# Optimization experiments

Measured on AMD Instinct MI355X. Metric: run time of the kernel, lower is better.

## Reference

```python
import jax, jax.numpy as jnp
import numpy as np

N = 50000
E = 800000
EPS = 1e-12


def sage_conv(x, src, dst, W_l, b_l, W_r):
    # PyG SAGEConv (mean aggr): out = lin_l(mean_{j in N(i)} x_j) + lin_r(x_i)
    msg = x[src]                                             # [E, d] gather
    agg = jax.ops.segment_sum(msg, dst, num_segments=N)      # [N, d]
    cnt = jax.ops.segment_sum(jnp.ones((E,), x.dtype), dst, num_segments=N)
    mean = agg / jnp.maximum(cnt, 1.0)[:, None]              # isolated nodes -> 0
    return mean @ W_l + b_l + x @ W_r


def setup_inputs() -> dict:
    key = jax.random.key(0)
    ks = jax.random.split(key, 12)
    s = 0.05
    return {
        "x": jax.random.normal(ks[0], (N, 128), dtype=jnp.float32),
        "edge_index": jax.random.randint(ks[1], (2, E), 0, N, dtype=jnp.int64),
        # pre: Linear(128 -> 128)
        "pre_W": jax.random.normal(ks[2], (128, 128), dtype=jnp.float32) * s,
        "pre_b": jnp.zeros((128,), dtype=jnp.float32),
        # conv_first: SAGEConv(128 -> 256)
        "W1_l": jax.random.normal(ks[3], (128, 256), dtype=jnp.float32) * s,
        "b1": jnp.zeros((256,), dtype=jnp.float32),
        "W1_r": jax.random.normal(ks[4], (128, 256), dtype=jnp.float32) * s,
        # conv_hidden[0]: SAGEConv(256 -> 256)
        "W2_l": jax.random.normal(ks[5], (256, 256), dtype=jnp.float32) * s,
        "b2": jnp.zeros((256,), dtype=jnp.float32),
        "W2_r": jax.random.normal(ks[6], (256, 256), dtype=jnp.float32) * s,
        # conv_out: SAGEConv(256 -> 256)
        "W3_l": jax.random.normal(ks[7], (256, 256), dtype=jnp.float32) * s,
        "b3": jnp.zeros((256,), dtype=jnp.float32),
        "W3_r": jax.random.normal(ks[8], (256, 256), dtype=jnp.float32) * s,
    }


def reference(x, edge_index, pre_W, pre_b, W1_l, b1, W1_r, W2_l, b2, W2_r, W3_l, b3, W3_r):
    src, dst = edge_index[0], edge_index[1]
    h = x @ pre_W + pre_b                                   # feature_pre Linear
    h = jax.nn.relu(sage_conv(h, src, dst, W1_l, b1, W1_r))  # dropout = identity (eval)
    h = jax.nn.relu(sage_conv(h, src, dst, W2_l, b2, W2_r))
    h = sage_conv(h, src, dst, W3_l, b3, W3_r)
    norm = jnp.sqrt(jnp.sum(h * h, axis=-1, keepdims=True))
    return h / jnp.maximum(norm, EPS)                       # F.normalize(p=2, dim=-1)
```

## Files before the change

### kernel.cpp

```cpp
#include <hip/hip_runtime.h>
#include <cstddef>
#include <cstdint>


typedef __attribute__((ext_vector_type(8))) short short8;
typedef __attribute__((ext_vector_type(4))) float f32x4;

__device__ __forceinline__ unsigned rne_bf16(float f) {
    unsigned b = __float_as_uint(f);
    return (b + 0x7fffu + ((b >> 16) & 1u)) >> 16;
}
__device__ __forceinline__ float bf16_lo(unsigned u) { return __uint_as_float(u << 16); }
__device__ __forceinline__ float bf16_hi(unsigned u) { return __uint_as_float(u & 0xffff0000u); }


__global__ __launch_bounds__(256) void deg_kernel(const int* __restrict__ dst,
                                                  int* __restrict__ deg, int E) {
    int e = blockIdx.x * 256 + threadIdx.x;
    if (e < E) atomicAdd(&deg[dst[e]], 1);
}

__global__ __launch_bounds__(256) void bsum_kernel(const int* __restrict__ deg,
                                                   int* __restrict__ bsum, int n) {
    int i = blockIdx.x * 256 + threadIdx.x;
    int v = (i < n) ? deg[i] : 0;
#pragma unroll
    for (int s = 32; s > 0; s >>= 1) v += __shfl_down(v, s);
    __shared__ int ws[4];
    int lane = threadIdx.x & 63, w = threadIdx.x >> 6;
    if (lane == 0) ws[w] = v;
    __syncthreads();
    if (threadIdx.x == 0) bsum[blockIdx.x] = ws[0] + ws[1] + ws[2] + ws[3];
}

__global__ __launch_bounds__(256) void bscan_kernel(const int* __restrict__ bsum,
                                                    int* __restrict__ boff,
                                                    int* __restrict__ off,
                                                    int nb, int n, int E) {
    int t = threadIdx.x;
    int v = (t < nb) ? bsum[t] : 0;
    int incl = v;
#pragma unroll
    for (int s = 1; s < 64; s <<= 1) {
        int u = __shfl_up(incl, s);
        if ((t & 63) >= s) incl += u;
    }
    __shared__ int ws[4];
    int lane = t & 63, w = t >> 6;
    if (lane == 63) ws[w] = incl;
    __syncthreads();
    int woff = 0;
    for (int j = 0; j < w; ++j) woff += ws[j];
    if (t < nb) boff[t] = woff + incl - v;
    if (t == 0) off[n] = E;
}

__global__ __launch_bounds__(256) void scan_kernel(const int* __restrict__ deg,
                                                   const int* __restrict__ boff,
                                                   int* __restrict__ off,
                                                   float* __restrict__ inv, int n) {
    int i = blockIdx.x * 256 + threadIdx.x;
    int v = (i < n) ? deg[i] : 0;
    int incl = v;
#pragma unroll
    for (int s = 1; s < 64; s <<= 1) {
        int u = __shfl_up(incl, s);
        if ((threadIdx.x & 63) >= s) incl += u;
    }
    __shared__ int ws[4];
    int lane = threadIdx.x & 63, w = threadIdx.x >> 6;
    if (lane == 63) ws[w] = incl;
    __syncthreads();
    int woff = 0;
    for (int j = 0; j < w; ++j) woff += ws[j];
    if (i < n) {
        off[i] = boff[blockIdx.x] + woff + incl - v;
        inv[i] = 1.0f / fmaxf((float)v, 1.0f);
    }
}

__global__ __launch_bounds__(256) void fill_kernel(const int* __restrict__ src,
                                                   const int* __restrict__ dst,
                                                   const int* __restrict__ off,
                                                   int* __restrict__ deg,
                                                   int* __restrict__ ssrc, int E) {
    int e = blockIdx.x * 256 + threadIdx.x;
    if (e >= E) return;
    int d = dst[e];
    int pos = off[d] + atomicSub(&deg[d], 1) - 1;
    ssrc[pos] = src[e];
}


__global__ __launch_bounds__(256) void xconv(const float* __restrict__ x,
                                             uint2* __restrict__ xb, int n4) {
    int i = blockIdx.x * 256 + threadIdx.x;
    if (i >= n4) return;
    float4 v = ((const float4*)x)[i];
    uint2 o;
    o.x = rne_bf16(v.x) | (rne_bf16(v.y) << 16);
    o.y = rne_bf16(v.z) | (rne_bf16(v.w) << 16);
    xb[i] = o;
}

__global__ __launch_bounds__(256) void wprep(
    const float* __restrict__ pre_W, const float* __restrict__ W1_l,
    const float* __restrict__ W1_r, const float* __restrict__ W2_l,
    const float* __restrict__ W2_r, const float* __restrict__ W3_l,
    const float* __restrict__ W3_r,
    unsigned short* __restrict__ WT0, unsigned short* __restrict__ WT1,
    unsigned short* __restrict__ WT2, unsigned short* __restrict__ WT3,
    unsigned short* __restrict__ WT4, unsigned short* __restrict__ WT5,
    unsigned short* __restrict__ WT6) {
    int idx = blockIdx.x * 256 + threadIdx.x;
    if (idx < 16384) {
        int k = idx >> 7, n = idx & 127;
        WT0[n * 128 + k] = (unsigned short)rne_bf16(pre_W[idx]);
        return;
    }
    idx -= 16384;
    if (idx < 32768) {
        int k = idx >> 8, n = idx & 255;
        WT1[n * 128 + k] = (unsigned short)rne_bf16(W1_l[idx]);
        return;
    }
    idx -= 32768;
    if (idx < 32768) {
        int k = idx >> 8, n = idx & 255;
        WT2[n * 128 + k] = (unsigned short)rne_bf16(W1_r[idx]);
        return;
    }
    idx -= 32768;
    if (idx < 65536) {
        int k = idx >> 8, n = idx & 255;
        WT3[n * 256 + k] = (unsigned short)rne_bf16(W2_l[idx]);
        return;
    }
    idx -= 65536;
    if (idx < 65536) {
        int k = idx >> 8, n = idx & 255;
        WT4[n * 256 + k] = (unsigned short)rne_bf16(W2_r[idx]);
        return;
    }
    idx -= 65536;
    if (idx < 65536) {
        int k = idx >> 8, n = idx & 255;
        WT5[n * 256 + k] = (unsigned short)rne_bf16(W3_l[idx]);
        return;
    }
    idx -= 65536;
    if (idx < 65536) {
        int k = idx >> 8, n = idx & 255;
        WT6[n * 256 + k] = (unsigned short)rne_bf16(W3_r[idx]);
    }
}


template <int D>
__global__ __launch_bounds__(256) void gather_b(const unsigned short* __restrict__ h,
                                                const int* __restrict__ off,
                                                const int* __restrict__ ssrc,
                                                const float* __restrict__ inv,
                                                unsigned short* __restrict__ agg, int n) {
    int node = blockIdx.x * 4 + (threadIdx.x >> 6);
    if (node >= n) return;
    int lane = threadIdx.x & 63;
    int beg = off[node], end = off[node + 1];
    float sc = inv[node];

    if (D == 256) {
        const unsigned short* col = h + (lane << 2);
        float a0 = 0, a1 = 0, a2 = 0, a3 = 0;
        float b0 = 0, b1 = 0, b2 = 0, b3 = 0;
        int k = beg;
        for (; k + 1 < end; k += 2) {
            int s0 = ssrc[k], s1 = ssrc[k + 1];
            uint2 u = *(const uint2*)(col + (size_t)s0 * 256);
            uint2 v = *(const uint2*)(col + (size_t)s1 * 256);
            a0 += bf16_lo(u.x); a1 += bf16_hi(u.x);
            a2 += bf16_lo(u.y); a3 += bf16_hi(u.y);
            b0 += bf16_lo(v.x); b1 += bf16_hi(v.x);
            b2 += bf16_lo(v.y); b3 += bf16_hi(v.y);
        }
        if (k < end) {
            uint2 u = *(const uint2*)(col + (size_t)ssrc[k] * 256);
            a0 += bf16_lo(u.x); a1 += bf16_hi(u.x);
            a2 += bf16_lo(u.y); a3 += bf16_hi(u.y);
        }
        a0 = (a0 + b0) * sc; a1 = (a1 + b1) * sc;
        a2 = (a2 + b2) * sc; a3 = (a3 + b3) * sc;
        uint2 o;
        o.x = rne_bf16(a0) | (rne_bf16(a1) << 16);
        o.y = rne_bf16(a2) | (rne_bf16(a3) << 16);
        *(uint2*)(agg + (size_t)node * 256 + (lane << 2)) = o;
    } else {
        const unsigned short* col = h + (lane << 1);
        float a0 = 0, a1 = 0, b0 = 0, b1 = 0;
        int k = beg;
        for (; k + 1 < end; k += 2) {
            int s0 = ssrc[k], s1 = ssrc[k + 1];
            unsigned u = *(const unsigned*)(col + (size_t)s0 * 128);
            unsigned v = *(const unsigned*)(col + (size_t)s1 * 128);
            a0 += bf16_lo(u); a1 += bf16_hi(u);
            b0 += bf16_lo(v); b1 += bf16_hi(v);
        }
        if (k < end) {
            unsigned u = *(const unsigned*)(col + (size_t)ssrc[k] * 128);
            a0 += bf16_lo(u); a1 += bf16_hi(u);
        }
        a0 = (a0 + b0) * sc; a1 = (a1 + b1) * sc;
        *(unsigned*)(agg + (size_t)node * 128 + (lane << 1)) =
            rne_bf16(a0) | (rne_bf16(a1) << 16);
    }
}

__global__ __launch_bounds__(256) void gemm_bt(
    const unsigned short* __restrict__ A1, const unsigned short* __restrict__ W1T,
    const unsigned short* __restrict__ A2, const unsigned short* __restrict__ W2T,
    const float* __restrict__ bias,
    unsigned short* __restrict__ outb, float* __restrict__ outf,
    int M, int K, int Nn, int relu) {
    __shared__ __align__(16) unsigned short As[128 * 64];
    __shared__ __align__(16) unsigned short Bs[128 * 64];

    const int t = threadIdx.x;
    const int lane = t & 63;
    const int w = t >> 6;
    const int wm = w >> 1, wn = w & 1;
    const int m0 = blockIdx.x * 128;
    const int n0 = blockIdx.y * 128;

    f32x4 acc[4][4];
#pragma unroll
    for (int i = 0; i < 4; ++i)
#pragma unroll
        for (int j = 0; j < 4; ++j) acc[i][j] = (f32x4){0.f, 0.f, 0.f, 0.f};

    for (int pass = 0; pass < 2; ++pass) {
        const unsigned short* A = pass ? A2 : A1;
        const unsigned short* W = pass ? W2T : W1T;
        if (pass && A2 == nullptr) break;

        for (int k0 = 0; k0 < K; k0 += 64) {
#pragma unroll
            for (int r = 0; r < 4; ++r) {
                int p = r * 256 + t;
                int row = p >> 3, slot = p & 7;
                int c = slot ^ (row & 7);
                int gm = m0 + row;
                if (gm >= M) gm = M - 1;
                uint4 va = *(const uint4*)(A + (size_t)gm * K + k0 + c * 8);
                uint4 vb = *(const uint4*)(W + (size_t)(n0 + row) * K + k0 + c * 8);
                *(uint4*)&As[(size_t)p * 8] = va;
                *(uint4*)&Bs[(size_t)p * 8] = vb;
            }
            __syncthreads();
#pragma unroll
            for (int kk = 0; kk < 2; ++kk) {
                short8 af[4], bfr[4];
                int ac = kk * 4 + (lane >> 4);
#pragma unroll
                for (int i = 0; i < 4; ++i) {
                    int arow = wm * 64 + i * 16 + (lane & 15);
                    af[i] = *(const short8*)&As[arow * 64 + ((ac ^ (arow & 7)) << 3)];
                    int brow = wn * 64 + i * 16 + (lane & 15);
                    bfr[i] = *(const short8*)&Bs[brow * 64 + ((ac ^ (brow & 7)) << 3)];
                }
#pragma unroll
                for (int mi = 0; mi < 4; ++mi)
#pragma unroll
                    for (int ni = 0; ni < 4; ++ni)
                        acc[mi][ni] = __builtin_amdgcn_mfma_f32_16x16x32_bf16(
                            af[mi], bfr[ni], acc[mi][ni], 0, 0, 0);
            }
            __syncthreads();
        }
    }

#pragma unroll
    for (int ni = 0; ni < 4; ++ni) {
        int n = n0 + wn * 64 + ni * 16 + (lane & 15);
        float bv = (bias != nullptr) ? bias[n] : 0.0f;
#pragma unroll
        for (int mi = 0; mi < 4; ++mi) {
            int mbase = m0 + wm * 64 + mi * 16 + ((lane >> 4) << 2);
#pragma unroll
            for (int r = 0; r < 4; ++r) {
                int m = mbase + r;
                if (m >= M) continue;
                float v = acc[mi][ni][r] + bv;
                if (relu) v = fmaxf(v, 0.0f);
                if (outb) outb[(size_t)m * Nn + n] = (unsigned short)rne_bf16(v);
                else      outf[(size_t)m * Nn + n] = v;
            }
        }
    }
}

__global__ __launch_bounds__(256) void norm_kernel(float* __restrict__ out, int M) {
    int row  = blockIdx.x * 4 + (threadIdx.x >> 6);
    int lane = threadIdx.x & 63;
    if (row >= M) return;
    float4 v = *(float4*)(out + (size_t)row * 256 + (lane << 2));
    float s = v.x * v.x + v.y * v.y + v.z * v.z + v.w * v.w;
#pragma unroll
    for (int off = 32; off > 0; off >>= 1) s += __shfl_down(s, off);
    s = __shfl(s, 0);
    float scale = 1.0f / fmaxf(sqrtf(s), 1e-12f);
    v.x *= scale; v.y *= scale; v.z *= scale; v.w *= scale;
    *(float4*)(out + (size_t)row * 256 + (lane << 2)) = v;
}

extern "C" void kernel_launch(void* const* d_in, const int* in_sizes, int n_in,
                              void* d_out, int out_size, void* d_ws, size_t ws_size,
                              hipStream_t stream) {
    const int N = 50000;
    const int E = 800000;
    const int NB = (N + 255) / 256;

    const float* x     = (const float*)d_in[0];
    const int*   ei    = (const int*)d_in[1];
    const float* pre_W = (const float*)d_in[2];
    const float* pre_b = (const float*)d_in[3];
    const float* W1_l  = (const float*)d_in[4];
    const float* b1    = (const float*)d_in[5];
    const float* W1_r  = (const float*)d_in[6];
    const float* W2_l  = (const float*)d_in[7];
    const float* b2    = (const float*)d_in[8];
    const float* W2_r  = (const float*)d_in[9];
    const float* W3_l  = (const float*)d_in[10];
    const float* b3    = (const float*)d_in[11];
    const float* W3_r  = (const float*)d_in[12];
    float* out = (float*)d_out;

    const int* src = ei;
    const int* dst = ei + E;

    int* deg  = (int*)d_ws;
    int* off  = deg + N;
    int* bsum = off + N + 1;
    int* boff = bsum + 256;
    int* ssrc = boff + 256;
    size_t int_words = (size_t)2 * N + 1 + 512 + E;
    int_words = (int_words + 3) & ~(size_t)3;

    float* inv = (float*)d_ws + int_words;
    unsigned short* us = (unsigned short*)(inv + N);

    unsigned short* xb  = us;                 us += (size_t)N * 128;
    unsigned short* WT0 = us;                 us += 16384;
    unsigned short* WT1 = us;                 us += 32768;
    unsigned short* WT2 = us;                 us += 32768;
    unsigned short* WT3 = us;                 us += 65536;
    unsigned short* WT4 = us;                 us += 65536;
    unsigned short* WT5 = us;                 us += 65536;
    unsigned short* WT6 = us;                 us += 65536;
    unsigned short* h0b   = us;               us += (size_t)N * 128;
    unsigned short* agg1b = us;               us += (size_t)N * 128;
    unsigned short* h1b   = us;               us += (size_t)N * 256;
    unsigned short* agg2b = us;               us += (size_t)N * 256;
    unsigned short* h2b   = us;               us += (size_t)N * 256;
    unsigned short* agg3b = us;               us += (size_t)N * 256;

    hipMemsetAsync(deg, 0, (size_t)N * sizeof(int), stream);
    deg_kernel<<<(E + 255) / 256, 256, 0, stream>>>(dst, deg, E);
    bsum_kernel<<<NB, 256, 0, stream>>>(deg, bsum, N);
    bscan_kernel<<<1, 256, 0, stream>>>(bsum, boff, off, NB, N, E);
    scan_kernel<<<NB, 256, 0, stream>>>(deg, boff, off, inv, N);
    fill_kernel<<<(E + 255) / 256, 256, 0, stream>>>(src, dst, off, deg, ssrc, E);

    xconv<<<(N * 128 / 4 + 255) / 256, 256, 0, stream>>>(x, (uint2*)xb, N * 128 / 4);
    wprep<<<(344064 + 255) / 256, 256, 0, stream>>>(pre_W, W1_l, W1_r, W2_l, W2_r,
                                                    W3_l, W3_r, WT0, WT1, WT2, WT3,
                                                    WT4, WT5, WT6);

    const int MT = (N + 127) / 128;
    const int AG = (N + 3) / 4;

    gemm_bt<<<dim3(MT, 1), 256, 0, stream>>>(xb, WT0, nullptr, nullptr, pre_b,
                                             h0b, nullptr, N, 128, 128, 0);

    gather_b<128><<<AG, 256, 0, stream>>>(h0b, off, ssrc, inv, agg1b, N);
    gemm_bt<<<dim3(MT, 2), 256, 0, stream>>>(agg1b, WT1, h0b, WT2, b1,
                                             h1b, nullptr, N, 128, 256, 1);

    gather_b<256><<<AG, 256, 0, stream>>>(h1b, off, ssrc, inv, agg2b, N);
    gemm_bt<<<dim3(MT, 2), 256, 0, stream>>>(agg2b, WT3, h1b, WT4, b2,
                                             h2b, nullptr, N, 256, 256, 1);

    gather_b<256><<<AG, 256, 0, stream>>>(h2b, off, ssrc, inv, agg3b, N);
    gemm_bt<<<dim3(MT, 2), 256, 0, stream>>>(agg3b, WT5, h2b, WT6, b3,
                                             nullptr, out, N, 256, 256, 0);

    norm_kernel<<<AG, 256, 0, stream>>>(out, N);
}
```

Before: 547.9 us.

## Degree-sort nodes and gather multiple edges per wave with 16-byte loads

Adds a counting sort of nodes by in-degree (histogram, scan, fill) so waves in the same block handle nodes with similar edge counts, reducing load imbalance in the gather kernels. The gather kernels are rewritten so each lane loads 16 bytes (8 bf16) and different sub-groups of the wave process different edges concurrently, then combine partial sums via cross-lane shuffles. This raises memory-level parallelism per wave at the cost of three extra preprocessing kernels and a memset, and it scatters output writes in permuted node order.

```diff
diff --git a/kernel.cpp b/kernel.cpp
--- a/kernel.cpp
+++ b/kernel.cpp
@@ -12,6 +12,13 @@
 }
 __device__ __forceinline__ float bf16_lo(unsigned u) { return __uint_as_float(u << 16); }
 __device__ __forceinline__ float bf16_hi(unsigned u) { return __uint_as_float(u & 0xffff0000u); }
+
+__device__ __forceinline__ void add8(float* a, uint4 u) {
+    a[0] += bf16_lo(u.x); a[1] += bf16_hi(u.x);
+    a[2] += bf16_lo(u.y); a[3] += bf16_hi(u.y);
+    a[4] += bf16_lo(u.z); a[5] += bf16_hi(u.z);
+    a[6] += bf16_lo(u.w); a[7] += bf16_hi(u.w);
+}
 
 
 __global__ __launch_bounds__(256) void deg_kernel(const int* __restrict__ dst,
@@ -89,6 +96,46 @@
     int d = dst[e];
     int pos = off[d] + atomicSub(&deg[d], 1) - 1;
     ssrc[pos] = src[e];
+}
+
+
+__global__ __launch_bounds__(256) void dhist_kernel(const int* __restrict__ off,
+                                                    int* __restrict__ hist, int n) {
+    int v = blockIdx.x * 256 + threadIdx.x;
+    if (v < n) atomicAdd(&hist[min(off[v + 1] - off[v], 1023)], 1);
+}
+
+__global__ __launch_bounds__(256) void dscan_kernel(const int* __restrict__ hist,
+                                                    int* __restrict__ doff) {
+    int t = threadIdx.x;
+    int s0 = hist[t * 4], s1 = hist[t * 4 + 1], s2 = hist[t * 4 + 2], s3 = hist[t * 4 + 3];
+    int sum = s0 + s1 + s2 + s3;
+    int incl = sum;
+#pragma unroll
+    for (int s = 1; s < 64; s <<= 1) {
+        int u = __shfl_up(incl, s);
+        if ((t & 63) >= s) incl += u;
+    }
+    __shared__ int ws[4];
+    int lane = t & 63, w = t >> 6;
+    if (lane == 63) ws[w] = incl;
+    __syncthreads();
+    int woff = 0;
+    for (int j = 0; j < w; ++j) woff += ws[j];
+    int base = woff + incl - sum;
+    doff[t * 4]     = base;
+    doff[t * 4 + 1] = base + s0;
+    doff[t * 4 + 2] = base + s0 + s1;
+    doff[t * 4 + 3] = base + s0 + s1 + s2;
+}
+
+__global__ __launch_bounds__(256) void dfill_kernel(const int* __restrict__ off,
+                                                    int* __restrict__ doff,
+                                                    int* __restrict__ perm, int n) {
+    int v = blockIdx.x * 256 + threadIdx.x;
+    if (v >= n) return;
+    int d = min(off[v + 1] - off[v], 1023);
+    perm[atomicAdd(&doff[d], 1)] = v;
 }
 
 
@@ -155,62 +202,108 @@
     }
 }
 
-
-template <int D>
-__global__ __launch_bounds__(256) void gather_b(const unsigned short* __restrict__ h,
-                                                const int* __restrict__ off,
-                                                const int* __restrict__ ssrc,
-                                                const float* __restrict__ inv,
-                                                unsigned short* __restrict__ agg, int n) {
-    int node = blockIdx.x * 4 + (threadIdx.x >> 6);
-    if (node >= n) return;
+__global__ __launch_bounds__(256) void gather256(const unsigned short* __restrict__ h,
+                                                 const int* __restrict__ off,
+                                                 const int* __restrict__ ssrc,
+                                                 const float* __restrict__ inv,
+                                                 const int* __restrict__ perm,
+                                                 unsigned short* __restrict__ agg, int n) {
+    int idx = blockIdx.x * 4 + (threadIdx.x >> 6);
+    if (idx >= n) return;
+    int node = perm[idx];
     int lane = threadIdx.x & 63;
+    int half = lane >> 5;
+    int c = (lane & 31) << 3;
     int beg = off[node], end = off[node + 1];
     float sc = inv[node];
-
-    if (D == 256) {
-        const unsigned short* col = h + (lane << 2);
-        float a0 = 0, a1 = 0, a2 = 0, a3 = 0;
-        float b0 = 0, b1 = 0, b2 = 0, b3 = 0;
-        int k = beg;
-        for (; k + 1 < end; k += 2) {
-            int s0 = ssrc[k], s1 = ssrc[k + 1];
-            uint2 u = *(const uint2*)(col + (size_t)s0 * 256);
-            uint2 v = *(const uint2*)(col + (size_t)s1 * 256);
-            a0 += bf16_lo(u.x); a1 += bf16_hi(u.x);
-            a2 += bf16_lo(u.y); a3 += bf16_hi(u.y);
-            b0 += bf16_lo(v.x); b1 += bf16_hi(v.x);
-            b2 += bf16_lo(v.y); b3 += bf16_hi(v.y);
-        }
-        if (k < end) {
-            uint2 u = *(const uint2*)(col + (size_t)ssrc[k] * 256);
-            a0 += bf16_lo(u.x); a1 += bf16_hi(u.x);
-            a2 += bf16_lo(u.y); a3 += bf16_hi(u.y);
-        }
-        a0 = (a0 + b0) * sc; a1 = (a1 + b1) * sc;
-        a2 = (a2 + b2) * sc; a3 = (a3 + b3) * sc;
-        uint2 o;
-        o.x = rne_bf16(a0) | (rne_bf16(a1) << 16);
-        o.y = rne_bf16(a2) | (rne_bf16(a3) << 16);
-        *(uint2*)(agg + (size_t)node * 256 + (lane << 2)) = o;
-    } else {
-        const unsigned short* col = h + (lane << 1);
-        float a0 = 0, a1 = 0, b0 = 0, b1 = 0;
-        int k = beg;
-        for (; k + 1 < end; k += 2) {
-            int s0 = ssrc[k], s1 = ssrc[k + 1];
-            unsigned u = *(const unsigned*)(col + (size_t)s0 * 128);
-            unsigned v = *(const unsigned*)(col + (size_t)s1 * 128);
-            a0 += bf16_lo(u); a1 += bf16_hi(u);
-            b0 += bf16_lo(v); b1 += bf16_hi(v);
-        }
-        if (k < end) {
-            unsigned u = *(const unsigned*)(col + (size_t)ssrc[k] * 128);
-            a0 += bf16_lo(u); a1 += bf16_hi(u);
-        }
-        a0 = (a0 + b0) * sc; a1 = (a1 + b1) * sc;
-        *(unsigned*)(agg + (size_t)node * 128 + (lane << 1)) =
-            rne_bf16(a0) | (rne_bf16(a1) << 16);
+    const unsigned short* colp = h + c;
+
+    float a[8] = {0, 0, 0, 0, 0, 0, 0, 0};
+    float b[8] = {0, 0, 0, 0, 0, 0, 0, 0};
+    int k = beg;
+    for (; k + 3 < end; k += 4) {
+        int sA = ssrc[k + half];
+        int sB = ssrc[k + 2 + half];
+        uint4 u = *(const uint4*)(colp + (size_t)sA * 256);
+        uint4 v = *(const uint4*)(colp + (size_t)sB * 256);
+        add8(a, u);
+        add8(b, v);
+    }
+    if (k + 1 < end) {
+        uint4 u = *(const uint4*)(colp + (size_t)ssrc[k + half] * 256);
+        add8(a, u);
+        k += 2;
+    }
+    if (k < end && half == 0) {
+        uint4 u = *(const uint4*)(colp + (size_t)ssrc[k] * 256);
+        add8(a, u);
+    }
+#pragma unroll
+    for (int i = 0; i < 8; ++i) {
+        a[i] += b[i];
+        a[i] += __shfl_xor(a[i], 32);
+        a[i] *= sc;
+    }
+    if (half == 0) {
+        uint4 o;
+        o.x = rne_bf16(a[0]) | (rne_bf16(a[1]) << 16);
+        o.y = rne_bf16(a[2]) | (rne_bf16(a[3]) << 16);
+        o.z = rne_bf16(a[4]) | (rne_bf16(a[5]) << 16);
+        o.w = rne_bf16(a[6]) | (rne_bf16(a[7]) << 16);
+        *(uint4*)(agg + (size_t)node * 256 + c) = o;
+    }
+}
+
+__global__ __launch_bounds__(256) void gather128(const unsigned short* __restrict__ h,
+                                                 const int* __restrict__ off,
+                                                 const int* __restrict__ ssrc,
+                                                 const float* __restrict__ inv,
+                                                 const int* __restrict__ perm,
+                                                 unsigned short* __restrict__ agg, int n) {
+    int idx = blockIdx.x * 4 + (threadIdx.x >> 6);
+    if (idx >= n) return;
+    int node = perm[idx];
+    int lane = threadIdx.x & 63;
+    int q = lane >> 4;
+    int c = (lane & 15) << 3;
+    int beg = off[node], end = off[node + 1];
+    float sc = inv[node];
+    const unsigned short* colp = h + c;
+
+    float a[8] = {0, 0, 0, 0, 0, 0, 0, 0};
+    float b[8] = {0, 0, 0, 0, 0, 0, 0, 0};
+    int k = beg;
+    for (; k + 7 < end; k += 8) {
+        int sA = ssrc[k + q];
+        int sB = ssrc[k + 4 + q];
+        uint4 u = *(const uint4*)(colp + (size_t)sA * 128);
+        uint4 v = *(const uint4*)(colp + (size_t)sB * 128);
+        add8(a, u);
+        add8(b, v);
+    }
+    if (k + 3 < end) {
+        uint4 u = *(const uint4*)(colp + (size_t)ssrc[k + q] * 128);
+        add8(a, u);
+        k += 4;
+    }
+    if (q < end - k) {
+        uint4 u = *(const uint4*)(colp + (size_t)ssrc[k + q] * 128);
+        add8(a, u);
+    }
+#pragma unroll
+    for (int i = 0; i < 8; ++i) {
+        a[i] += b[i];
+        a[i] += __shfl_xor(a[i], 32);
+        a[i] += __shfl_xor(a[i], 16);
+        a[i] *= sc;
+    }
+    if (q == 0) {
+        uint4 o;
+        o.x = rne_bf16(a[0]) | (rne_bf16(a[1]) << 16);
+        o.y = rne_bf16(a[2]) | (rne_bf16(a[3]) << 16);
+        o.z = rne_bf16(a[4]) | (rne_bf16(a[5]) << 16);
+        o.w = rne_bf16(a[6]) | (rne_bf16(a[7]) << 16);
+        *(uint4*)(agg + (size_t)node * 128 + c) = o;
     }
 }
 
@@ -340,8 +433,11 @@
     int* off  = deg + N;
     int* bsum = off + N + 1;
     int* boff = bsum + 256;
-    int* ssrc = boff + 256;
-    size_t int_words = (size_t)2 * N + 1 + 512 + E;
+    int* hist = boff + 256;
+    int* doff = hist + 1024;
+    int* perm = doff + 1024;
+    int* ssrc = perm + N;
+    size_t int_words = (size_t)3 * N + 1 + 512 + 2048 + E;
     int_words = (int_words + 3) & ~(size_t)3;
 
     float* inv = (float*)d_ws + int_words;
@@ -363,12 +459,17 @@
     unsigned short* agg3b = us;               us += (size_t)N * 256;
 
     hipMemsetAsync(deg, 0, (size_t)N * sizeof(int), stream);
+    hipMemsetAsync(hist, 0, 1024 * sizeof(int), stream);
     deg_kernel<<<(E + 255) / 256, 256, 0, stream>>>(dst, deg, E);
     bsum_kernel<<<NB, 256, 0, stream>>>(deg, bsum, N);
     bscan_kernel<<<1, 256, 0, stream>>>(bsum, boff, off, NB, N, E);
     scan_kernel<<<NB, 256, 0, stream>>>(deg, boff, off, inv, N);
     fill_kernel<<<(E + 255) / 256, 256, 0, stream>>>(src, dst, off, deg, ssrc, E);
 
+    dhist_kernel<<<NB, 256, 0, stream>>>(off, hist, N);
+    dscan_kernel<<<1, 256, 0, stream>>>(hist, doff);
+    dfill_kernel<<<NB, 256, 0, stream>>>(off, doff, perm, N);
+
     xconv<<<(N * 128 / 4 + 255) / 256, 256, 0, stream>>>(x, (uint2*)xb, N * 128 / 4);
     wprep<<<(344064 + 255) / 256, 256, 0, stream>>>(pre_W, W1_l, W1_r, W2_l, W2_r,
                                                     W3_l, W3_r, WT0, WT1, WT2, WT3,
@@ -380,15 +481,15 @@
     gemm_bt<<<dim3(MT, 1), 256, 0, stream>>>(xb, WT0, nullptr, nullptr, pre_b,
                                              h0b, nullptr, N, 128, 128, 0);
 
-    gather_b<128><<<AG, 256, 0, stream>>>(h0b, off, ssrc, inv, agg1b, N);
+    gather128<<<AG, 256, 0, stream>>>(h0b, off, ssrc, inv, perm, agg1b, N);
     gemm_bt<<<dim3(MT, 2), 256, 0, stream>>>(agg1b, WT1, h0b, WT2, b1,
                                              h1b, nullptr, N, 128, 256, 1);
 
-    gather_b<256><<<AG, 256, 0, stream>>>(h1b, off, ssrc, inv, agg2b, N);
+    gather256<<<AG, 256, 0, stream>>>(h1b, off, ssrc, inv, perm, agg2b, N);
     gemm_bt<<<dim3(MT, 2), 256, 0, stream>>>(agg2b, WT3, h1b, WT4, b2,
                                              h2b, nullptr, N, 256, 256, 1);
 
-    gather_b<256><<<AG, 256, 0, stream>>>(h2b, off, ssrc, inv, agg3b, N);
+    gather256<<<AG, 256, 0, stream>>>(h2b, off, ssrc, inv, perm, agg3b, N);
     gemm_bt<<<dim3(MT, 2), 256, 0, stream>>>(agg3b, WT5, h2b, WT6, b3,
                                              nullptr, out, N, 256, 256, 0);
 
```

After: 815.9 us. 1.49x slower.
